# Performance work log

Measured on AMD Instinct MI355X. Metric: run time of the kernel, lower is better.

Reference implementation:

```python
import jax
import jax.numpy as jnp
import numpy as np

SIGMA = 0.5
COLLISION_WEIGHT = 100.0
CE_WEIGHTS = (1.0, 30.0, 30.0, 10.0)
B, V, F, P = 512, 778, 1538, 1024


def _cone_field(tri, pts):
    # Conical distance field of receiver triangle `tri` [B,P,3,3] evaluated at
    # intruder vertices `pts` [B,P,3,3] (Tzionas et al. penetration field,
    # penalize_outside=False, point2plane=False). Returns [B,P].
    c = tri.mean(axis=-2)                                   # triangle center [B,P,3]
    n = jnp.cross(tri[..., 1, :] - tri[..., 0, :], tri[..., 2, :] - tri[..., 0, :])
    n = n / (jnp.linalg.norm(n, axis=-1, keepdims=True) + 1e-9)
    d = pts - c[..., None, :]                               # [B,P,3,3]
    h = jnp.einsum('bpvc,bpc->bpv', d, n)                   # signed height along normal
    rho2 = jnp.maximum(jnp.sum(d * d, axis=-1) - h * h, 0.0)  # squared radial dist
    phi = jax.nn.relu(-h) * jnp.exp(-rho2 / (2.0 * SIGMA * SIGMA))
    return phi.sum(axis=-1)


def _pen_distance(triangles, collision_idxs):
    # triangles [B,2F,3,3]; collision_idxs [B,P,2] with -1 padding -> per-batch loss [B]
    bb = jnp.arange(triangles.shape[0])[:, None]
    valid = (collision_idxs[..., 0] >= 0) & (collision_idxs[..., 1] >= 0)
    idx = jnp.maximum(collision_idxs, 0)
    recv = triangles[bb, idx[..., 0]]                       # [B,P,3,3]
    intr = triangles[bb, idx[..., 1]]
    pair = _cone_field(recv, intr) + _cone_field(intr, recv)
    return jnp.sum(pair * valid, axis=1)


def _collision_loss(out_vertices, faces, collision_idxs):
    nv = out_vertices.shape[2]
    verts = jnp.concatenate([out_vertices[0], out_vertices[1]], axis=1)   # [B,2V,3]
    faces_comb = jnp.concatenate([faces[0], faces[1] + nv], axis=0)       # [2F,3]
    triangles = verts[:, faces_comb]                                      # [B,2F,3,3]
    loss_b = _pen_distance(triangles, collision_idxs)
    nz = (loss_b != 0).astype(loss_b.dtype)
    cnt = nz.sum()
    return jnp.where(cnt > 0, (loss_b * nz).sum() / jnp.maximum(cnt, 1.0) * COLLISION_WEIGHT, 0.0)


def _index_loss(elem, mask):
    # masked mean exactly as Loss.index_losss: sum(loss*mask)/ (mask.sum()*D), 0 if empty
    l = elem.reshape(elem.shape[0], -1)
    denom = mask.sum() * l.shape[1]
    return jnp.where(denom > 0, (l * mask[:, None]).sum() / jnp.maximum(denom, 1.0), 0.0)


def _mse(a, b):
    return (a - b) ** 2


def _l1(a, b):
    return jnp.abs(a - b)


def setup_inputs():
    key = jax.random.key(0)
    ks = jax.random.split(key, 20)
    f32 = jnp.float32
    out_vertices = jax.random.normal(ks[0], (2, B, V, 3), f32) * 0.05
    out_betas = jax.random.normal(ks[1], (2, B, 10), f32)
    out_transl = jax.random.normal(ks[2], (2, B, 3), f32) * 0.1
    out_j3d = jax.random.normal(ks[3], (2, B, 21, 3), f32) * 0.1
    out_go = jax.random.normal(ks[4], (2, B, 3), f32)
    out_pose = jax.random.normal(ks[5], (2, B, 45), f32)
    tgt_trans = jax.random.normal(ks[6], (2, B, 3), f32) * 0.1
    tgt_j3d = jax.random.normal(ks[7], (2, B, 21, 3), f32) * 0.1
    tgt_go = jax.random.normal(ks[8], (2, B, 3), f32)
    tgt_pose = jax.random.normal(ks[9], (2, B, 45), f32)
    tgt_shape = jax.random.normal(ks[10], (2, B, 10), f32)
    class_logits = jax.random.normal(ks[11], (B, 4), f32)
    faces = jax.random.randint(ks[12], (2, F, 3), 0, V, jnp.int32)
    ci = jax.random.randint(ks[13], (B, P, 2), 0, 2 * F, jnp.int32)
    keep = jax.random.uniform(ks[14], (B, P, 1)) < 0.7
    collision_idxs = jnp.where(keep, ci, -1)
    handedness = jax.random.randint(ks[15], (B, 2), 0, 2, jnp.int32)
    valid = jax.random.randint(ks[16], (2, B), 0, 2, jnp.int32)
    class_targets = jax.random.randint(ks[17], (B,), 0, 4, jnp.int32)
    return dict(out_vertices=out_vertices, out_betas=out_betas, out_transl=out_transl,
                out_j3d=out_j3d, out_go=out_go, out_pose=out_pose, tgt_trans=tgt_trans,
                tgt_j3d=tgt_j3d, tgt_go=tgt_go, tgt_pose=tgt_pose, tgt_shape=tgt_shape,
                class_logits=class_logits, faces=faces, collision_idxs=collision_idxs,
                handedness=handedness, valid=valid, class_targets=class_targets)


def reference(out_vertices, out_betas, out_transl, out_j3d, out_go, out_pose,
              tgt_trans, tgt_j3d, tgt_go, tgt_pose, tgt_shape, class_logits,
              faces, collision_idxs, handedness, valid, class_targets):
    f32 = out_vertices.dtype
    loss_interpen = _collision_loss(out_vertices, faces, collision_idxs)
    inter = (handedness.sum(axis=1) == 2).astype(f32)
    loss_inter_shape = _index_loss(_mse(out_betas[0], out_betas[1]), inter)
    loss_inter_transl = _index_loss(_mse(out_transl[0] - out_transl[1],
                                         tgt_trans[0] - tgt_trans[1]), inter) * 100.0
    loss_inter_j3d = _index_loss(_mse(out_j3d[0] - out_j3d[1],
                                      tgt_j3d[0] - tgt_j3d[1]), inter) * 100.0
    lgo = lhp = lrj = lj3 = lsh = ltr = reg = jnp.zeros((), f32)
    for h in range(2):  # left, right
        m = valid[h].astype(f32)
        lgo = lgo + _index_loss(_mse(out_go[h], tgt_go[h]), m) * 10.0
        lhp = lhp + _index_loss(_mse(out_pose[h], tgt_pose[h]), m) * 10.0
        lrj = lrj + _index_loss(_l1((out_j3d[h][:, 1:] - out_j3d[h][:, :1]) * 1000.0,
                                    (tgt_j3d[h][:, 1:] - tgt_j3d[h][:, :1]) * 1000.0), m) * 0.01
        lj3 = lj3 + _index_loss(_l1(out_j3d[h] * 1000.0, tgt_j3d[h] * 1000.0), m) * 0.01
        lsh = lsh + _index_loss(_mse(out_betas[h], tgt_shape[h]), m) * 10.0
        ltr = ltr + _index_loss(_l1(out_transl[h], tgt_trans[h]), m) * 10.0
        reg = reg + 0.1 * _index_loss(_mse(out_betas[h], out_betas[h]), m)
        reg = reg + _index_loss(_mse(out_pose[h], out_pose[h]), m)
    # weighted cross entropy with ignore_index=0 (torch semantics)
    logp = jax.nn.log_softmax(class_logits, axis=-1)
    nll = -jnp.take_along_axis(logp, class_targets[:, None], axis=1)[:, 0]
    w = jnp.asarray(CE_WEIGHTS, f32)[class_targets]
    vmask = (class_targets != 0).astype(f32)
    ce = jnp.sum(w * vmask * nll) / jnp.maximum(jnp.sum(w * vmask), 1e-9)
    return jnp.stack([loss_interpen, loss_inter_shape, loss_inter_transl, loss_inter_j3d,
                      lgo, lhp, lrj, lj3, lsh, ltr, reg, ce])
```

## Files before the change

kernel.cpp:

```cpp
#include <hip/hip_runtime.h>
#include <math.h>

#define BB 512
#define VV 778
#define FF 1538
#define PP 1024
#define NS 16

__device__ __forceinline__ float cone3(const float3 t[3], const float3 p[3]) {
    const float third = 1.0f / 3.0f;
    float cx = (t[0].x + t[1].x + t[2].x) * third;
    float cy = (t[0].y + t[1].y + t[2].y) * third;
    float cz = (t[0].z + t[1].z + t[2].z) * third;
    float e1x = t[1].x - t[0].x, e1y = t[1].y - t[0].y, e1z = t[1].z - t[0].z;
    float e2x = t[2].x - t[0].x, e2y = t[2].y - t[0].y, e2z = t[2].z - t[0].z;
    float nx = e1y * e2z - e1z * e2y;
    float ny = e1z * e2x - e1x * e2z;
    float nz = e1x * e2y - e1y * e2x;
    float inv = 1.0f / (sqrtf(nx * nx + ny * ny + nz * nz) + 1e-9f);
    nx *= inv; ny *= inv; nz *= inv;
    float s = 0.0f;
#pragma unroll
    for (int i = 0; i < 3; i++) {
        float dx = p[i].x - cx, dy = p[i].y - cy, dz = p[i].z - cz;
        float h = dx * nx + dy * ny + dz * nz;
        float r2 = fmaxf(dx * dx + dy * dy + dz * dz - h * h, 0.0f);
        float rl = fmaxf(-h, 0.0f);
        s += rl * expf(-2.0f * r2);
    }
    return s;
}

__device__ __forceinline__ void loadTri(const int* __restrict__ faces,
                                        const float* __restrict__ sv,
                                        int f, float3 t[3]) {
    int off = (f >= FF) ? (VV * 3) : 0;
    const int* fp = faces + f * 3;
#pragma unroll
    for (int k = 0; k < 3; k++) {
        int j = fp[k] * 3 + off;
        t[k] = make_float3(sv[j], sv[j + 1], sv[j + 2]);
    }
}

__global__ __launch_bounds__(256) void per_batch_kernel(
    const float* __restrict__ verts,
    const int*   __restrict__ faces,
    const int*   __restrict__ cidx,
    const float* __restrict__ betas,
    const float* __restrict__ transl,
    const float* __restrict__ j3d,
    const float* __restrict__ go,
    const float* __restrict__ pose,
    const float* __restrict__ tgt_trans,
    const float* __restrict__ tgt_j3d,
    const float* __restrict__ tgt_go,
    const float* __restrict__ tgt_pose,
    const float* __restrict__ tgt_shape,
    float* __restrict__ ws)
{
    __shared__ float sv[2 * VV * 3];
    __shared__ float red[4][NS];
    const int b = blockIdx.x, tid = threadIdx.x;

    const float* v0 = verts + (size_t)b * VV * 3;
    const float* v1 = verts + (size_t)(BB + b) * VV * 3;
    for (int i = tid; i < VV * 3; i += 256) {
        sv[i] = v0[i];
        sv[VV * 3 + i] = v1[i];
    }
    __syncthreads();

    float part[NS];
#pragma unroll
    for (int k = 0; k < NS; k++) part[k] = 0.0f;

    const int2* ci = (const int2*)cidx + (size_t)b * PP;
    for (int p = tid; p < PP; p += 256) {
        int2 fp = ci[p];
        if (fp.x < 0 || fp.y < 0) continue;
        float3 r[3], q[3];
        loadTri(faces, sv, fp.x, r);
        loadTri(faces, sv, fp.y, q);
        part[0] += cone3(r, q) + cone3(q, r);
    }

    if (tid < 63) {
        const int t = tid;
        if (t < 10) { float d = betas[b * 10 + t] - betas[(BB + b) * 10 + t]; part[1] = d * d; }
        if (t < 3) {
            float d = (transl[b * 3 + t] - transl[(BB + b) * 3 + t]) -
                      (tgt_trans[b * 3 + t] - tgt_trans[(BB + b) * 3 + t]);
            part[2] = d * d;
        }
        {
            float d = (j3d[b * 63 + t] - j3d[(BB + b) * 63 + t]) -
                      (tgt_j3d[b * 63 + t] - tgt_j3d[(BB + b) * 63 + t]);
            part[3] = d * d;
        }
#pragma unroll
        for (int h = 0; h < 2; h++) {
            const int base = 4 + 6 * h;
            const size_t ob = (size_t)(h * BB + b);
            if (t < 3)  { float d = go[ob * 3 + t] - tgt_go[ob * 3 + t]; part[base + 0] = d * d; }
            if (t < 45) { float d = pose[ob * 45 + t] - tgt_pose[ob * 45 + t]; part[base + 1] = d * d; }
            if (t < 60) {
                int j = 1 + t / 3, c = t % 3;
                float a  = (j3d[ob * 63 + j * 3 + c]     - j3d[ob * 63 + c]) * 1000.0f;
                float b2 = (tgt_j3d[ob * 63 + j * 3 + c] - tgt_j3d[ob * 63 + c]) * 1000.0f;
                part[base + 2] = fabsf(a - b2);
            }
            {
                float a = j3d[ob * 63 + t] * 1000.0f, b2 = tgt_j3d[ob * 63 + t] * 1000.0f;
                part[base + 3] = fabsf(a - b2);
            }
            if (t < 10) { float d = betas[ob * 10 + t] - tgt_shape[ob * 10 + t]; part[base + 4] = d * d; }
            if (t < 3)  { float d = transl[ob * 3 + t] - tgt_trans[ob * 3 + t]; part[base + 5] = fabsf(d); }
        }
    }

#pragma unroll
    for (int off = 32; off >= 1; off >>= 1) {
#pragma unroll
        for (int k = 0; k < NS; k++) part[k] += __shfl_down(part[k], off);
    }
    const int wave = tid >> 6, lane = tid & 63;
    if (lane == 0) {
#pragma unroll
        for (int k = 0; k < NS; k++) red[wave][k] = part[k];
    }
    __syncthreads();
    if (tid < NS) {
        ws[b * NS + tid] = red[0][tid] + red[1][tid] + red[2][tid] + red[3][tid];
    }
}

__global__ __launch_bounds__(256) void finalize_kernel(
    const float* __restrict__ ws,
    const int*   __restrict__ handed,
    const int*   __restrict__ validm,
    const float* __restrict__ logits,
    const int*   __restrict__ ctgt,
    float* __restrict__ out)
{
    const int tid = threadIdx.x;
    const int NA = 22;
    float acc[22];
#pragma unroll
    for (int k = 0; k < NA; k++) acc[k] = 0.0f;

    for (int b = tid; b < BB; b += 256) {
        const float* w = ws + b * NS;
        float lb = w[0];
        acc[0] += lb;
        acc[1] += (lb != 0.0f) ? 1.0f : 0.0f;
        float inter = ((handed[b * 2] + handed[b * 2 + 1]) == 2) ? 1.0f : 0.0f;
        acc[2] += inter * w[1];
        acc[3] += inter * w[2];
        acc[4] += inter * w[3];
        acc[5] += inter;
#pragma unroll
        for (int h = 0; h < 2; h++) {
            float vm = (float)validm[h * BB + b];
            const int ab = 6 + 7 * h;
#pragma unroll
            for (int k = 0; k < 6; k++) acc[ab + k] += vm * w[4 + 6 * h + k];
            acc[ab + 6] += vm;
        }
        float l0 = logits[b * 4 + 0], l1 = logits[b * 4 + 1];
        float l2 = logits[b * 4 + 2], l3 = logits[b * 4 + 3];
        float m = fmaxf(fmaxf(l0, l1), fmaxf(l2, l3));
        float lse = m + logf(expf(l0 - m) + expf(l1 - m) + expf(l2 - m) + expf(l3 - m));
        int t = ctgt[b];
        float lt = (t == 0) ? l0 : (t == 1) ? l1 : (t == 2) ? l2 : l3;
        float nll = lse - lt;
        float cw = (t == 0) ? 1.0f : (t == 3) ? 10.0f : 30.0f;
        float vm = (t != 0) ? 1.0f : 0.0f;
        acc[20] += cw * vm * nll;
        acc[21] += cw * vm;
    }

#pragma unroll
    for (int off = 32; off >= 1; off >>= 1) {
#pragma unroll
        for (int k = 0; k < NA; k++) acc[k] += __shfl_down(acc[k], off);
    }
    __shared__ float red[4][22];
    const int wave = tid >> 6, lane = tid & 63;
    if (lane == 0) {
#pragma unroll
        for (int k = 0; k < NA; k++) red[wave][k] = acc[k];
    }
    __syncthreads();

    if (tid == 0) {
        float s[22];
#pragma unroll
        for (int k = 0; k < NA; k++)
            s[k] = red[0][k] + red[1][k] + red[2][k] + red[3][k];

        auto idxloss = [](float num, float cnt, float K) -> float {
            float denom = cnt * K;
            return (denom > 0.0f) ? num / fmaxf(denom, 1.0f) : 0.0f;
        };

        out[0] = (s[1] > 0.0f) ? s[0] / fmaxf(s[1], 1.0f) * 100.0f : 0.0f;
        out[1] = idxloss(s[2], s[5], 10.0f);
        out[2] = idxloss(s[3], s[5], 3.0f) * 100.0f;
        out[3] = idxloss(s[4], s[5], 63.0f) * 100.0f;
        out[4] = (idxloss(s[6],  s[12], 3.0f)  + idxloss(s[13], s[19], 3.0f))  * 10.0f;
        out[5] = (idxloss(s[7],  s[12], 45.0f) + idxloss(s[14], s[19], 45.0f)) * 10.0f;
        out[6] = (idxloss(s[8],  s[12], 60.0f) + idxloss(s[15], s[19], 60.0f)) * 0.01f;
        out[7] = (idxloss(s[9],  s[12], 63.0f) + idxloss(s[16], s[19], 63.0f)) * 0.01f;
        out[8] = (idxloss(s[10], s[12], 10.0f) + idxloss(s[17], s[19], 10.0f)) * 10.0f;
        out[9] = (idxloss(s[11], s[12], 3.0f)  + idxloss(s[18], s[19], 3.0f))  * 10.0f;
        out[10] = 0.0f;
        out[11] = s[20] / fmaxf(s[21], 1e-9f);
    }
}

extern "C" void kernel_launch(void* const* d_in, const int* in_sizes, int n_in,
                              void* d_out, int out_size, void* d_ws, size_t ws_size,
                              hipStream_t stream) {
    const float* verts   = (const float*)d_in[0];
    const float* betas   = (const float*)d_in[1];
    const float* transl  = (const float*)d_in[2];
    const float* j3d     = (const float*)d_in[3];
    const float* go      = (const float*)d_in[4];
    const float* pose    = (const float*)d_in[5];
    const float* tt      = (const float*)d_in[6];
    const float* tj      = (const float*)d_in[7];
    const float* tg      = (const float*)d_in[8];
    const float* tp      = (const float*)d_in[9];
    const float* tsh     = (const float*)d_in[10];
    const float* logits  = (const float*)d_in[11];
    const int*   faces   = (const int*)d_in[12];
    const int*   cidx    = (const int*)d_in[13];
    const int*   handed  = (const int*)d_in[14];
    const int*   validm  = (const int*)d_in[15];
    const int*   ctgt    = (const int*)d_in[16];
    float*       ws      = (float*)d_ws;
    float*       out     = (float*)d_out;

    per_batch_kernel<<<BB, 256, 0, stream>>>(verts, faces, cidx, betas, transl,
                                             j3d, go, pose, tt, tj, tg, tp, tsh, ws);
    finalize_kernel<<<1, 256, 0, stream>>>(ws, handed, validm, logits, ctgt, out);
}
```

Before: 109.2 us.

## Split per-batch kernel into four blocks per batch over collision pairs

Each batch is now handled by four blocks, one per quarter of the 1024 collision pairs, so each thread evaluates a single pair. Only the first block computes the small per-batch regression losses, using one wave and 15 accumulators instead of 16 reduced across every wave. Vertices are staged into shared memory with float2 loads, expf is replaced by exp2f with a prescaled constant, and launch bounds request higher occupancy. The cost is that every batch's vertices (about 18 KB) are loaded into shared memory four times, and finalize must sum four partial collision values per batch.

```diff
diff --git a/kernel.cpp b/kernel.cpp
--- a/kernel.cpp
+++ b/kernel.cpp
@@ -5,7 +5,9 @@
 #define VV 778
 #define FF 1538
 #define PP 1024
+#define PC 4
 #define NS 16
+
 
 __device__ __forceinline__ float cone3(const float3 t[3], const float3 p[3]) {
     const float third = 1.0f / 3.0f;
@@ -26,7 +28,7 @@
         float h = dx * nx + dy * ny + dz * nz;
         float r2 = fmaxf(dx * dx + dy * dy + dz * dz - h * h, 0.0f);
         float rl = fmaxf(-h, 0.0f);
-        s += rl * expf(-2.0f * r2);
+        s += rl * exp2f(-2.8853900817779268f * r2);
     }
     return s;
 }
@@ -43,7 +45,7 @@
     }
 }
 
-__global__ __launch_bounds__(256) void per_batch_kernel(
+__global__ __launch_bounds__(256, 8) void per_batch_kernel(
     const float* __restrict__ verts,
     const int*   __restrict__ faces,
     const int*   __restrict__ cidx,
@@ -60,78 +62,85 @@
     float* __restrict__ ws)
 {
     __shared__ float sv[2 * VV * 3];
-    __shared__ float red[4][NS];
-    const int b = blockIdx.x, tid = threadIdx.x;
-
-    const float* v0 = verts + (size_t)b * VV * 3;
-    const float* v1 = verts + (size_t)(BB + b) * VV * 3;
-    for (int i = tid; i < VV * 3; i += 256) {
-        sv[i] = v0[i];
-        sv[VV * 3 + i] = v1[i];
+    __shared__ float red[4];
+    const int bc = blockIdx.x;
+    const int b = bc >> 2, c = bc & (PC - 1);
+    const int tid = threadIdx.x;
+
+    const float2* v0 = (const float2*)(verts + (size_t)b * VV * 3);
+    const float2* v1 = (const float2*)(verts + (size_t)(BB + b) * VV * 3);
+    float2* s0 = (float2*)sv;
+    float2* s1 = (float2*)(sv + VV * 3);
+    for (int i = tid; i < VV * 3 / 2; i += 256) {
+        s0[i] = v0[i];
+        s1[i] = v1[i];
     }
     __syncthreads();
 
-    float part[NS];
-#pragma unroll
-    for (int k = 0; k < NS; k++) part[k] = 0.0f;
-
-    const int2* ci = (const int2*)cidx + (size_t)b * PP;
-    for (int p = tid; p < PP; p += 256) {
-        int2 fp = ci[p];
-        if (fp.x < 0 || fp.y < 0) continue;
-        float3 r[3], q[3];
-        loadTri(faces, sv, fp.x, r);
-        loadTri(faces, sv, fp.y, q);
-        part[0] += cone3(r, q) + cone3(q, r);
-    }
-
-    if (tid < 63) {
-        const int t = tid;
-        if (t < 10) { float d = betas[b * 10 + t] - betas[(BB + b) * 10 + t]; part[1] = d * d; }
-        if (t < 3) {
-            float d = (transl[b * 3 + t] - transl[(BB + b) * 3 + t]) -
-                      (tgt_trans[b * 3 + t] - tgt_trans[(BB + b) * 3 + t]);
-            part[2] = d * d;
-        }
-        {
-            float d = (j3d[b * 63 + t] - j3d[(BB + b) * 63 + t]) -
-                      (tgt_j3d[b * 63 + t] - tgt_j3d[(BB + b) * 63 + t]);
-            part[3] = d * d;
-        }
-#pragma unroll
-        for (int h = 0; h < 2; h++) {
-            const int base = 4 + 6 * h;
-            const size_t ob = (size_t)(h * BB + b);
-            if (t < 3)  { float d = go[ob * 3 + t] - tgt_go[ob * 3 + t]; part[base + 0] = d * d; }
-            if (t < 45) { float d = pose[ob * 45 + t] - tgt_pose[ob * 45 + t]; part[base + 1] = d * d; }
-            if (t < 60) {
-                int j = 1 + t / 3, c = t % 3;
-                float a  = (j3d[ob * 63 + j * 3 + c]     - j3d[ob * 63 + c]) * 1000.0f;
-                float b2 = (tgt_j3d[ob * 63 + j * 3 + c] - tgt_j3d[ob * 63 + c]) * 1000.0f;
-                part[base + 2] = fabsf(a - b2);
+    float coll = 0.0f;
+    {
+        const int p = c * 256 + tid;
+        int2 fp = ((const int2*)cidx)[(size_t)b * PP + p];
+        if (fp.x >= 0 && fp.y >= 0) {
+            float3 r[3], q[3];
+            loadTri(faces, sv, fp.x, r);
+            loadTri(faces, sv, fp.y, q);
+            coll = cone3(r, q) + cone3(q, r);
+        }
+    }
+#pragma unroll
+    for (int off = 32; off >= 1; off >>= 1) coll += __shfl_down(coll, off);
+    const int wave = tid >> 6, lane = tid & 63;
+    if (lane == 0) red[wave] = coll;
+    __syncthreads();
+    if (tid == 0) ws[8192 + b * PC + c] = red[0] + red[1] + red[2] + red[3];
+
+    if (c == 0 && tid < 64) {
+        float sl[15];
+#pragma unroll
+        for (int k = 0; k < 15; k++) sl[k] = 0.0f;
+        if (tid < 63) {
+            const int t = tid;
+            if (t < 10) { float d = betas[b * 10 + t] - betas[(BB + b) * 10 + t]; sl[0] = d * d; }
+            if (t < 3) {
+                float d = (transl[b * 3 + t] - transl[(BB + b) * 3 + t]) -
+                          (tgt_trans[b * 3 + t] - tgt_trans[(BB + b) * 3 + t]);
+                sl[1] = d * d;
             }
             {
-                float a = j3d[ob * 63 + t] * 1000.0f, b2 = tgt_j3d[ob * 63 + t] * 1000.0f;
-                part[base + 3] = fabsf(a - b2);
+                float d = (j3d[b * 63 + t] - j3d[(BB + b) * 63 + t]) -
+                          (tgt_j3d[b * 63 + t] - tgt_j3d[(BB + b) * 63 + t]);
+                sl[2] = d * d;
             }
-            if (t < 10) { float d = betas[ob * 10 + t] - tgt_shape[ob * 10 + t]; part[base + 4] = d * d; }
-            if (t < 3)  { float d = transl[ob * 3 + t] - tgt_trans[ob * 3 + t]; part[base + 5] = fabsf(d); }
-        }
-    }
-
-#pragma unroll
-    for (int off = 32; off >= 1; off >>= 1) {
-#pragma unroll
-        for (int k = 0; k < NS; k++) part[k] += __shfl_down(part[k], off);
-    }
-    const int wave = tid >> 6, lane = tid & 63;
-    if (lane == 0) {
-#pragma unroll
-        for (int k = 0; k < NS; k++) red[wave][k] = part[k];
-    }
-    __syncthreads();
-    if (tid < NS) {
-        ws[b * NS + tid] = red[0][tid] + red[1][tid] + red[2][tid] + red[3][tid];
+#pragma unroll
+            for (int h = 0; h < 2; h++) {
+                const int base = 3 + 6 * h;
+                const size_t ob = (size_t)(h * BB + b);
+                if (t < 3)  { float d = go[ob * 3 + t] - tgt_go[ob * 3 + t]; sl[base + 0] = d * d; }
+                if (t < 45) { float d = pose[ob * 45 + t] - tgt_pose[ob * 45 + t]; sl[base + 1] = d * d; }
+                if (t < 60) {
+                    int j = 1 + t / 3, cc = t % 3;
+                    float a  = (j3d[ob * 63 + j * 3 + cc]     - j3d[ob * 63 + cc]) * 1000.0f;
+                    float b2 = (tgt_j3d[ob * 63 + j * 3 + cc] - tgt_j3d[ob * 63 + cc]) * 1000.0f;
+                    sl[base + 2] = fabsf(a - b2);
+                }
+                {
+                    float a = j3d[ob * 63 + t] * 1000.0f, b2 = tgt_j3d[ob * 63 + t] * 1000.0f;
+                    sl[base + 3] = fabsf(a - b2);
+                }
+                if (t < 10) { float d = betas[ob * 10 + t] - tgt_shape[ob * 10 + t]; sl[base + 4] = d * d; }
+                if (t < 3)  { float d = transl[ob * 3 + t] - tgt_trans[ob * 3 + t]; sl[base + 5] = fabsf(d); }
+            }
+        }
+#pragma unroll
+        for (int off = 32; off >= 1; off >>= 1) {
+#pragma unroll
+            for (int k = 0; k < 15; k++) sl[k] += __shfl_down(sl[k], off);
+        }
+        if (tid == 0) {
+#pragma unroll
+            for (int k = 0; k < 15; k++) ws[b * NS + 1 + k] = sl[k];
+        }
     }
 }
 
@@ -151,7 +160,8 @@
 
     for (int b = tid; b < BB; b += 256) {
         const float* w = ws + b * NS;
-        float lb = w[0];
+        float lb = ws[8192 + b * PC + 0] + ws[8192 + b * PC + 1] +
+                   ws[8192 + b * PC + 2] + ws[8192 + b * PC + 3];
         acc[0] += lb;
         acc[1] += (lb != 0.0f) ? 1.0f : 0.0f;
         float inter = ((handed[b * 2] + handed[b * 2 + 1]) == 2) ? 1.0f : 0.0f;
@@ -242,7 +252,7 @@
     float*       ws      = (float*)d_ws;
     float*       out     = (float*)d_out;
 
-    per_batch_kernel<<<BB, 256, 0, stream>>>(verts, faces, cidx, betas, transl,
-                                             j3d, go, pose, tt, tj, tg, tp, tsh, ws);
+    per_batch_kernel<<<BB * PC, 256, 0, stream>>>(verts, faces, cidx, betas, transl,
+                                                  j3d, go, pose, tt, tj, tg, tp, tsh, ws);
     finalize_kernel<<<1, 256, 0, stream>>>(ws, handed, validm, logits, ctgt, out);
 }
```

Result: no change. 110.4 us (+1.1%).
